# Kernel tuning notes

Hardware: AMD Instinct MI355X
Metric: run time of the kernel (lower is better)

Reference implementation:

```python
import jax, jax.numpy as jnp
import numpy as np

B, S, C, H, D = 2, 2048, 1024, 16, 64  # hidden C must equal H*D (value is a reshape of key_states)


def setup_inputs() -> dict:
    key = jax.random.key(0)
    ks = jax.random.split(key, 7)
    query_states = jax.random.normal(ks[0], (B, S, C), dtype=jnp.float32)
    key_states = jax.random.normal(ks[1], (B, S, C), dtype=jnp.float32)
    attention_mask = jax.random.randint(ks[2], (B, 1, 1, S), 0, 2).astype(jnp.int32)
    Wq = jax.random.normal(ks[3], (C, H, D), dtype=jnp.float32) * 0.02
    bq = jnp.zeros((H, D), dtype=jnp.float32)
    Wk = jax.random.normal(ks[4], (C, H, D), dtype=jnp.float32) * 0.02
    bk = jnp.zeros((H, D), dtype=jnp.float32)
    return {
        "query_states": query_states,
        "key_states": key_states,
        "attention_mask": attention_mask,
        "Wq": Wq,
        "bq": bq,
        "Wk": Wk,
        "bk": bk,
    }


def reference(query_states, key_states, attention_mask, Wq, bq, Wk, bk):
    # EinsumDense 'abc,cde->abde' with bias on 'de'
    q = jnp.einsum("bsc,chd->bshd", query_states, Wq) + bq  # [B,S,H,D]
    k = jnp.einsum("bsc,chd->bshd", key_states, Wk) + bk    # [B,S,H,D]
    # value is just key_states reshaped into head layout (no projection!)
    v = key_states.reshape(k.shape)                          # [B,S,H,D]
    # scale query by 1/sqrt(dk)
    q = q * jax.lax.rsqrt(jnp.asarray(D, q.dtype))
    # 'aecd,abcd->acbe': a=batch, c=head, b=query pos, e=key pos
    scores = jnp.einsum("bkhd,bqhd->bhqk", k, q)             # [B,H,Sq,Sk]
    mask = (1.0 - attention_mask.astype(scores.dtype)) * -10000.0
    scores = scores + mask
    probs = jax.nn.softmax(scores, axis=-1)
    # dropout is identity at training=False (default)
    # 'acbe,aecd->abcd': weighted sum of values over key positions
    out = jnp.einsum("bhqk,bkhd->bqhd", probs, v)            # [B,S,H,D]
    return out
```

## Files before the change

### kernel.cpp

```cpp
#include <hip/hip_runtime.h>

#define BSZ 2
#define SEQ 2048
#define CH  1024
#define NH  16
#define HD  64
#define LOG2E 1.4426950408889634f
#define MASKC (-14426.950408889634f)

typedef short  bf16x8 __attribute__((ext_vector_type(8)));
typedef short  bf16x4 __attribute__((ext_vector_type(4)));
typedef float  f32x4  __attribute__((ext_vector_type(4)));

__device__ __forceinline__ short f2bf(float f) {
    union { float f; unsigned u; } v; v.f = f;
    unsigned r = v.u + 0x7FFFu + ((v.u >> 16) & 1u);
    return (short)(r >> 16);
}
__device__ __forceinline__ short f2bf_fast(float f) {
    union { float f; unsigned u; } v; v.f = f;
    return (short)((v.u + 0x8000u) >> 16);
}
__device__ __forceinline__ float exp2_hw(float x) {
#if __has_builtin(__builtin_amdgcn_exp2f)
    return __builtin_amdgcn_exp2f(x);
#else
    float r;
    asm volatile("v_exp_f32 %0, %1\n\ts_nop 1" : "=v"(r) : "v"(x));
    return r;
#endif
}

#if __has_builtin(__builtin_amdgcn_mfma_f32_16x16x16bf16_1k)
__device__ __forceinline__ f32x4 mfma16x16x16(bf16x4 a, bf16x4 b, f32x4 c) {
    return __builtin_amdgcn_mfma_f32_16x16x16bf16_1k(a, b, c, 0, 0, 0);
}
#else
__device__ __forceinline__ f32x4 mfma16x16x16(bf16x4 a, bf16x4 b, f32x4 c) {
    f32x4 d;
    asm("v_mfma_f32_16x16x16_bf16 %0, %1, %2, %3"
        : "=v"(d) : "v"(a), "v"(b), "v"(c));
    return d;
}
#endif

__global__ __launch_bounds__(256) void prep(
    const float* __restrict__ query, const float* __restrict__ key,
    const float* __restrict__ Wq, const float* __restrict__ Wk,
    short* __restrict__ qc, short* __restrict__ kc,
    short* __restrict__ wtq, short* __restrict__ wtk,
    short* __restrict__ vtr)
{
    __shared__ float tile[64][65];
    const int bid = blockIdx.x;
    const int tid = threadIdx.x;

    if (bid < 4096) {
        const float* s = (bid < 2048) ? query : key;
        short*       d = (bid < 2048) ? qc : kc;
        long i = ((long)(bid & 2047) * 256 + tid) * 8;
        float4 v0 = *(const float4*)&s[i];
        float4 v1 = *(const float4*)&s[i + 4];
        bf16x8 o;
        o[0] = f2bf(v0.x); o[1] = f2bf(v0.y); o[2] = f2bf(v0.z); o[3] = f2bf(v0.w);
        o[4] = f2bf(v1.x); o[5] = f2bf(v1.y); o[6] = f2bf(v1.z); o[7] = f2bf(v1.w);
        *(bf16x8*)&d[i] = o;
        return;
    }

    const float* s; short* d;
    int r0, c0, srs, drs;
    if (bid < 4608) {
        int t = bid - 4096;
        s   = (t < 256) ? Wq : Wk;
        d   = (t < 256) ? wtq : wtk;
        t  &= 255;
        r0  = (t >> 4) * 64;
        c0  = (t & 15) * 64;
        srs = CH; drs = CH;
    } else {
        int t = bid - 4608;
        int z = t >> 5;
        int sy = t & 31;
        s   = key + (long)(z >> 4) * SEQ * CH + (long)(z & 15) * HD;
        d   = vtr + (long)z * HD * SEQ;
        r0  = sy * 64;
        c0  = 0;
        srs = CH; drs = SEQ;
    }

    const int r  = tid >> 2;
    const int c4 = (tid & 3) << 4;
    #pragma unroll
    for (int i = 0; i < 16; i += 4) {
        float4 v = *(const float4*)&s[(long)(r0 + r) * srs + c0 + c4 + i];
        tile[r][c4 + i + 0] = v.x;
        tile[r][c4 + i + 1] = v.y;
        tile[r][c4 + i + 2] = v.z;
        tile[r][c4 + i + 3] = v.w;
    }
    __syncthreads();
    bf16x8 o0, o1;
    #pragma unroll
    for (int i = 0; i < 8; i++) o0[i] = f2bf(tile[c4 + i][r]);
    #pragma unroll
    for (int i = 0; i < 8; i++) o1[i] = f2bf(tile[c4 + 8 + i][r]);
    *(bf16x8*)&d[(long)(c0 + r) * drs + r0 + c4 + 0] = o0;
    *(bf16x8*)&d[(long)(c0 + r) * drs + r0 + c4 + 8] = o1;
}

__global__ __launch_bounds__(256, 2) void proj_mfma(
    const short* __restrict__ Xq, const short* __restrict__ Xk,
    const short* __restrict__ Wtq, const short* __restrict__ Wtk,
    const float* __restrict__ bq_, const float* __restrict__ bk_,
    short* __restrict__ Yq, short* __restrict__ Yk)
{
    __shared__ short At[2][128 * 72];
    __shared__ short Bt[2][128 * 72];
    const int zz = blockIdx.z;
    const short* X    = zz ? Xk  : Xq;
    const short* Wt   = zz ? Wtk : Wtq;
    const float* bias = zz ? bk_ : bq_;
    short*       Y    = zz ? Yk  : Yq;
    const float scale = zz ? 1.0f : (0.125f * LOG2E);

    const int tid  = threadIdx.x;
    const int lane = tid & 63, w = tid >> 6;
    const int quad = lane >> 4, t16 = lane & 15;
    const int m0 = blockIdx.y * 128, n0 = blockIdx.x * 128;
    const int srow = tid >> 1;
    const int shalf = (tid & 1) * 32;

    f32x4 acc[4][4];
    #pragma unroll
    for (int i = 0; i < 4; i++)
        #pragma unroll
        for (int j = 0; j < 4; j++)
            acc[i][j] = (f32x4){0.f, 0.f, 0.f, 0.f};

    const int M0 = (w >> 1) * 64, N0 = (w & 1) * 64;
    const int NIT = CH / 64;

    bf16x8 ar[4], br[4];
    #pragma unroll
    for (int c = 0; c < 4; c++) {
        ar[c] = *(const bf16x8*)&X [(long)(m0 + srow) * CH + shalf + 8 * c];
        br[c] = *(const bf16x8*)&Wt[(long)(n0 + srow) * CH + shalf + 8 * c];
    }
    #pragma unroll
    for (int c = 0; c < 4; c++) {
        *(bf16x8*)&At[0][srow * 72 + shalf + 8 * c] = ar[c];
        *(bf16x8*)&Bt[0][srow * 72 + shalf + 8 * c] = br[c];
    }
    #pragma unroll
    for (int c = 0; c < 4; c++) {
        ar[c] = *(const bf16x8*)&X [(long)(m0 + srow) * CH + 64 + shalf + 8 * c];
        br[c] = *(const bf16x8*)&Wt[(long)(n0 + srow) * CH + 64 + shalf + 8 * c];
    }
    __syncthreads();

    for (int it = 0; it < NIT; it++) {
        const int buf = it & 1;
        if (it + 1 < NIT) {
            #pragma unroll
            for (int c = 0; c < 4; c++) {
                *(bf16x8*)&At[buf ^ 1][srow * 72 + shalf + 8 * c] = ar[c];
                *(bf16x8*)&Bt[buf ^ 1][srow * 72 + shalf + 8 * c] = br[c];
            }
            if (it + 2 < NIT) {
                const long ko = (long)(it + 2) * 64;
                #pragma unroll
                for (int c = 0; c < 4; c++) {
                    ar[c] = *(const bf16x8*)&X [(long)(m0 + srow) * CH + ko + shalf + 8 * c];
                    br[c] = *(const bf16x8*)&Wt[(long)(n0 + srow) * CH + ko + shalf + 8 * c];
                }
            }
        }

        #pragma unroll
        for (int kk = 0; kk < 2; kk++) {
            bf16x8 af[4], bw[4];
            #pragma unroll
            for (int im = 0; im < 4; im++)
                af[im] = *(bf16x8*)&At[buf][(M0 + 16 * im + t16) * 72 + kk * 32 + quad * 8];
            #pragma unroll
            for (int jn = 0; jn < 4; jn++)
                bw[jn] = *(bf16x8*)&Bt[buf][(N0 + 16 * jn + t16) * 72 + kk * 32 + quad * 8];
            #pragma unroll
            for (int im = 0; im < 4; im++)
                #pragma unroll
                for (int jn = 0; jn < 4; jn++)
                    acc[im][jn] = __builtin_amdgcn_mfma_f32_16x16x32_bf16(
                        af[im], bw[jn], acc[im][jn], 0, 0, 0);
        }
        __syncthreads();
    }

    #pragma unroll
    for (int jn = 0; jn < 4; jn++) {
        float bs = bias[n0 + N0 + 16 * jn + t16];
        #pragma unroll
        for (int im = 0; im < 4; im++)
            #pragma unroll
            for (int reg = 0; reg < 4; reg++) {
                float y = (acc[im][jn][reg] + bs) * scale;
                Y[(long)(m0 + M0 + 16 * im + 4 * quad + reg) * (NH * HD)
                  + n0 + N0 + 16 * jn + t16] = f2bf(y);
            }
    }
}

__global__ __launch_bounds__(256, 2) void attn_mfma(
    const short* __restrict__ qp,
    const short* __restrict__ kp,
    const short* __restrict__ vt,
    const int*   __restrict__ amask,
    float* __restrict__ out)
{
    __shared__ short Kt[2][64 * 72];
    __shared__ short Vt[2][64 * 72];

    const int qt0 = blockIdx.x * 128;
    const int h   = blockIdx.y;
    const int b   = blockIdx.z;
    const int tid = threadIdx.x;
    const int lane = tid & 63, w = tid >> 6;
    const int quad = lane >> 4, t16 = lane & 15;

    bf16x8 qf[2][2];
    #pragma unroll
    for (int qm = 0; qm < 2; qm++)
        #pragma unroll
        for (int ds = 0; ds < 2; ds++)
            qf[qm][ds] = *(const bf16x8*)&qp[
                (long)(b * SEQ + qt0 + w * 32 + qm * 16 + t16) * CH
                + h * HD + ds * 32 + quad * 8];

    f32x4 oa[4][2];
    float l_r[2];
    #pragma unroll
    for (int dt = 0; dt < 4; dt++)
        #pragma unroll
        for (int qm = 0; qm < 2; qm++)
            oa[dt][qm] = (f32x4){0.f, 0.f, 0.f, 0.f};
    l_r[0] = l_r[1] = 0.f;

    const int srow  = tid >> 2;
    const int scol  = (tid & 3) * 16;
    const long kbase = (long)(b * SEQ) * CH + h * HD;
    const long vbase = ((long)(b * NH + h) * HD) * SEQ;
    const int NIT = SEQ / 64;

    bf16x8 kr[2], vr[2];
    #pragma unroll
    for (int c = 0; c < 2; c++) {
        kr[c] = *(const bf16x8*)&kp[kbase + (long)srow * CH + scol + 8 * c];
        vr[c] = *(const bf16x8*)&vt[vbase + (long)srow * SEQ + scol + 8 * c];
    }
    #pragma unroll
    for (int c = 0; c < 2; c++) {
        *(bf16x8*)&Kt[0][srow * 72 + scol + 8 * c] = kr[c];
        *(bf16x8*)&Vt[0][srow * 72 + scol + 8 * c] = vr[c];
    }
    #pragma unroll
    for (int c = 0; c < 2; c++) {
        kr[c] = *(const bf16x8*)&kp[kbase + (long)(64 + srow) * CH + scol + 8 * c];
        vr[c] = *(const bf16x8*)&vt[vbase + (long)srow * SEQ + 64 + scol + 8 * c];
    }
    __syncthreads();

    for (int it = 0; it < NIT; it++) {
        const int buf = it & 1;
        const int kt0 = it * 64;

        if (it + 1 < NIT) {
            #pragma unroll
            for (int c = 0; c < 2; c++) {
                *(bf16x8*)&Kt[buf ^ 1][srow * 72 + scol + 8 * c] = kr[c];
                *(bf16x8*)&Vt[buf ^ 1][srow * 72 + scol + 8 * c] = vr[c];
            }
            if (it + 2 < NIT) {
                const int kn = kt0 + 128;
                #pragma unroll
                for (int c = 0; c < 2; c++) {
                    kr[c] = *(const bf16x8*)&kp[kbase + (long)(kn + srow) * CH + scol + 8 * c];
                    vr[c] = *(const bf16x8*)&vt[vbase + (long)srow * SEQ + kn + scol + 8 * c];
                }
            }
        }

        float4 mv4[4];
        #pragma unroll
        for (int jt = 0; jt < 4; jt++) {
            int4 a4 = *(const int4*)&amask[b * SEQ + kt0 + jt * 16 + quad * 4];
            mv4[jt].x = a4.x ? 0.f : MASKC;
            mv4[jt].y = a4.y ? 0.f : MASKC;
            mv4[jt].z = a4.z ? 0.f : MASKC;
            mv4[jt].w = a4.w ? 0.f : MASKC;
        }

        f32x4 sa[2][4];
        #pragma unroll
        for (int qm = 0; qm < 2; qm++)
            #pragma unroll
            for (int jt = 0; jt < 4; jt++)
                sa[qm][jt] = (f32x4){mv4[jt].x, mv4[jt].y, mv4[jt].z, mv4[jt].w};
        #pragma unroll
        for (int ds = 0; ds < 2; ds++) {
            bf16x8 kb[4];
            #pragma unroll
            for (int jt = 0; jt < 4; jt++)
                kb[jt] = *(bf16x8*)&Kt[buf][(jt * 16 + t16) * 72 + ds * 32 + quad * 8];
            #pragma unroll
            for (int qm = 0; qm < 2; qm++)
                #pragma unroll
                for (int jt = 0; jt < 4; jt++)
                    sa[qm][jt] = __builtin_amdgcn_mfma_f32_16x16x32_bf16(
                        kb[jt], qf[qm][ds], sa[qm][jt], 0, 0, 0);
        }

        bf16x4 pb[2][4];
        #pragma unroll
        for (int qm = 0; qm < 2; qm++)
            #pragma unroll
            for (int jt = 0; jt < 4; jt++) {
                float p0 = exp2_hw(sa[qm][jt][0]);
                float p1 = exp2_hw(sa[qm][jt][1]);
                float p2 = exp2_hw(sa[qm][jt][2]);
                float p3 = exp2_hw(sa[qm][jt][3]);
                l_r[qm] += (p0 + p1) + (p2 + p3);
                bf16x4 pk;
                pk[0] = f2bf_fast(p0); pk[1] = f2bf_fast(p1);
                pk[2] = f2bf_fast(p2); pk[3] = f2bf_fast(p3);
                pb[qm][jt] = pk;
            }

        #pragma unroll
        for (int jt = 0; jt < 4; jt++) {
            bf16x4 va[4];
            #pragma unroll
            for (int dt = 0; dt < 4; dt++)
                va[dt] = *(bf16x4*)&Vt[buf][(dt * 16 + t16) * 72 + jt * 16 + quad * 4];
            #pragma unroll
            for (int dt = 0; dt < 4; dt++)
                #pragma unroll
                for (int qm = 0; qm < 2; qm++)
                    oa[dt][qm] = mfma16x16x16(va[dt], pb[qm][jt], oa[dt][qm]);
        }
        __syncthreads();
    }

    #pragma unroll
    for (int qm = 0; qm < 2; qm++) {
        float l = l_r[qm];
        l += __shfl_xor(l, 16, 64);
        l += __shfl_xor(l, 32, 64);
        float inv = 1.0f / l;
        int q = qt0 + w * 32 + qm * 16 + t16;
        #pragma unroll
        for (int dt = 0; dt < 4; dt++) {
            f32x4 o = oa[dt][qm];
            float4 st = {o[0] * inv, o[1] * inv, o[2] * inv, o[3] * inv};
            *(float4*)&out[((long)(b * SEQ + q) * NH + h) * HD + dt * 16 + quad * 4] = st;
        }
    }
}

extern "C" void kernel_launch(void* const* d_in, const int* in_sizes, int n_in,
                              void* d_out, int out_size, void* d_ws, size_t ws_size,
                              hipStream_t stream) {
    const float* query = (const float*)d_in[0];
    const float* key   = (const float*)d_in[1];
    const int*   amask = (const int*)d_in[2];
    const float* Wq    = (const float*)d_in[3];
    const float* bq    = (const float*)d_in[4];
    const float* Wk    = (const float*)d_in[5];
    const float* bk    = (const float*)d_in[6];
    float* out = (float*)d_out;

    char* ws = (char*)d_ws;
    const long MB = 1024 * 1024;
    short* qc  = (short*)(ws + 0 * MB);
    short* kc  = (short*)(ws + 8 * MB);
    short* qp  = (short*)(ws + 16 * MB);
    short* kp  = (short*)(ws + 24 * MB);
    short* vtr = (short*)(ws + 32 * MB);
    short* wtq = (short*)(ws + 40 * MB);
    short* wtk = (short*)(ws + 42 * MB);

    prep<<<dim3(5632), 256, 0, stream>>>(query, key, Wq, Wk, qc, kc, wtq, wtk, vtr);

    dim3 pgrid((NH * HD) / 128, (BSZ * SEQ) / 128, 2);
    proj_mfma<<<pgrid, 256, 0, stream>>>(qc, kc, wtq, wtk, bq, bk, qp, kp);

    dim3 agrid(SEQ / 128, NH, BSZ);
    attn_mfma<<<agrid, 256, 0, stream>>>(qp, kp, vtr, amask, out);
}
```

Measured before the change: 174.8 us.

## Fuse fp32-to-bf16 input conversion into projection GEMM and precompute float mask

```diff
diff --git a/kernel.cpp b/kernel.cpp
--- a/kernel.cpp
+++ b/kernel.cpp
@@ -20,6 +20,12 @@
 __device__ __forceinline__ short f2bf_fast(float f) {
     union { float f; unsigned u; } v; v.f = f;
     return (short)((v.u + 0x8000u) >> 16);
+}
+__device__ __forceinline__ bf16x8 pack8(float4 a, float4 b) {
+    bf16x8 o;
+    o[0] = f2bf(a.x); o[1] = f2bf(a.y); o[2] = f2bf(a.z); o[3] = f2bf(a.w);
+    o[4] = f2bf(b.x); o[5] = f2bf(b.y); o[6] = f2bf(b.z); o[7] = f2bf(b.w);
+    return o;
 }
 __device__ __forceinline__ float exp2_hw(float x) {
 #if __has_builtin(__builtin_amdgcn_exp2f)
@@ -45,33 +51,26 @@
 #endif
 
 __global__ __launch_bounds__(256) void prep(
-    const float* __restrict__ query, const float* __restrict__ key,
+    const float* __restrict__ key,
     const float* __restrict__ Wq, const float* __restrict__ Wk,
-    short* __restrict__ qc, short* __restrict__ kc,
+    const int*   __restrict__ am,
     short* __restrict__ wtq, short* __restrict__ wtk,
-    short* __restrict__ vtr)
+    short* __restrict__ vtr, float* __restrict__ mf)
 {
     __shared__ float tile[64][65];
     const int bid = blockIdx.x;
     const int tid = threadIdx.x;
 
-    if (bid < 4096) {
-        const float* s = (bid < 2048) ? query : key;
-        short*       d = (bid < 2048) ? qc : kc;
-        long i = ((long)(bid & 2047) * 256 + tid) * 8;
-        float4 v0 = *(const float4*)&s[i];
-        float4 v1 = *(const float4*)&s[i + 4];
-        bf16x8 o;
-        o[0] = f2bf(v0.x); o[1] = f2bf(v0.y); o[2] = f2bf(v0.z); o[3] = f2bf(v0.w);
-        o[4] = f2bf(v1.x); o[5] = f2bf(v1.y); o[6] = f2bf(v1.z); o[7] = f2bf(v1.w);
-        *(bf16x8*)&d[i] = o;
+    if (bid >= 1536) {
+        int i = (bid - 1536) * 256 + tid;
+        mf[i] = (1.0f - (float)am[i]) * MASKC * (1.0f / 1.0f);
         return;
     }
 
     const float* s; short* d;
     int r0, c0, srs, drs;
-    if (bid < 4608) {
-        int t = bid - 4096;
+    if (bid < 512) {
+        int t = bid;
         s   = (t < 256) ? Wq : Wk;
         d   = (t < 256) ? wtq : wtk;
         t  &= 255;
@@ -79,7 +78,7 @@
         c0  = (t & 15) * 64;
         srs = CH; drs = CH;
     } else {
-        int t = bid - 4608;
+        int t = bid - 512;
         int z = t >> 5;
         int sy = t & 31;
         s   = key + (long)(z >> 4) * SEQ * CH + (long)(z & 15) * HD;
@@ -110,7 +109,7 @@
 }
 
 __global__ __launch_bounds__(256, 2) void proj_mfma(
-    const short* __restrict__ Xq, const short* __restrict__ Xk,
+    const float* __restrict__ Xq, const float* __restrict__ Xk,
     const short* __restrict__ Wtq, const short* __restrict__ Wtk,
     const float* __restrict__ bq_, const float* __restrict__ bk_,
     short* __restrict__ Yq, short* __restrict__ Yk)
@@ -118,7 +117,7 @@
     __shared__ short At[2][128 * 72];
     __shared__ short Bt[2][128 * 72];
     const int zz = blockIdx.z;
-    const short* X    = zz ? Xk  : Xq;
+    const float* X    = zz ? Xk  : Xq;
     const short* Wt   = zz ? Wtk : Wtq;
     const float* bias = zz ? bk_ : bq_;
     short*       Y    = zz ? Yk  : Yq;
@@ -141,22 +140,25 @@
     const int M0 = (w >> 1) * 64, N0 = (w & 1) * 64;
     const int NIT = CH / 64;
 
-    bf16x8 ar[4], br[4];
+    float4 xr[8];
+    bf16x8 br[4];
+    #pragma unroll
+    for (int c = 0; c < 8; c++)
+        xr[c] = *(const float4*)&X[(long)(m0 + srow) * CH + shalf + 4 * c];
+    #pragma unroll
+    for (int c = 0; c < 4; c++)
+        br[c] = *(const bf16x8*)&Wt[(long)(n0 + srow) * CH + shalf + 8 * c];
     #pragma unroll
     for (int c = 0; c < 4; c++) {
-        ar[c] = *(const bf16x8*)&X [(long)(m0 + srow) * CH + shalf + 8 * c];
-        br[c] = *(const bf16x8*)&Wt[(long)(n0 + srow) * CH + shalf + 8 * c];
-    }
-    #pragma unroll
-    for (int c = 0; c < 4; c++) {
-        *(bf16x8*)&At[0][srow * 72 + shalf + 8 * c] = ar[c];
+        *(bf16x8*)&At[0][srow * 72 + shalf + 8 * c] = pack8(xr[2 * c], xr[2 * c + 1]);
         *(bf16x8*)&Bt[0][srow * 72 + shalf + 8 * c] = br[c];
     }
     #pragma unroll
-    for (int c = 0; c < 4; c++) {
-        ar[c] = *(const bf16x8*)&X [(long)(m0 + srow) * CH + 64 + shalf + 8 * c];
+    for (int c = 0; c < 8; c++)
+        xr[c] = *(const float4*)&X[(long)(m0 + srow) * CH + 64 + shalf + 4 * c];
+    #pragma unroll
+    for (int c = 0; c < 4; c++)
         br[c] = *(const bf16x8*)&Wt[(long)(n0 + srow) * CH + 64 + shalf + 8 * c];
-    }
     __syncthreads();
 
     for (int it = 0; it < NIT; it++) {
@@ -164,16 +166,17 @@
         if (it + 1 < NIT) {
             #pragma unroll
             for (int c = 0; c < 4; c++) {
-                *(bf16x8*)&At[buf ^ 1][srow * 72 + shalf + 8 * c] = ar[c];
+                *(bf16x8*)&At[buf ^ 1][srow * 72 + shalf + 8 * c] = pack8(xr[2 * c], xr[2 * c + 1]);
                 *(bf16x8*)&Bt[buf ^ 1][srow * 72 + shalf + 8 * c] = br[c];
             }
             if (it + 2 < NIT) {
                 const long ko = (long)(it + 2) * 64;
                 #pragma unroll
-                for (int c = 0; c < 4; c++) {
-                    ar[c] = *(const bf16x8*)&X [(long)(m0 + srow) * CH + ko + shalf + 8 * c];
+                for (int c = 0; c < 8; c++)
+                    xr[c] = *(const float4*)&X[(long)(m0 + srow) * CH + ko + shalf + 4 * c];
+                #pragma unroll
+                for (int c = 0; c < 4; c++)
                     br[c] = *(const bf16x8*)&Wt[(long)(n0 + srow) * CH + ko + shalf + 8 * c];
-                }
             }
         }
 
@@ -214,7 +217,7 @@
     const short* __restrict__ qp,
     const short* __restrict__ kp,
     const short* __restrict__ vt,
-    const int*   __restrict__ amask,
+    const float* __restrict__ mf,
     float* __restrict__ out)
 {
     __shared__ short Kt[2][64 * 72];
@@ -291,13 +294,8 @@
 
         float4 mv4[4];
         #pragma unroll
-        for (int jt = 0; jt < 4; jt++) {
-            int4 a4 = *(const int4*)&amask[b * SEQ + kt0 + jt * 16 + quad * 4];
-            mv4[jt].x = a4.x ? 0.f : MASKC;
-            mv4[jt].y = a4.y ? 0.f : MASKC;
-            mv4[jt].z = a4.z ? 0.f : MASKC;
-            mv4[jt].w = a4.w ? 0.f : MASKC;
-        }
+        for (int jt = 0; jt < 4; jt++)
+            mv4[jt] = *(const float4*)&mf[b * SEQ + kt0 + jt * 16 + quad * 4];
 
         f32x4 sa[2][4];
         #pragma unroll
@@ -380,19 +378,18 @@
 
     char* ws = (char*)d_ws;
     const long MB = 1024 * 1024;
-    short* qc  = (short*)(ws + 0 * MB);
-    short* kc  = (short*)(ws + 8 * MB);
-    short* qp  = (short*)(ws + 16 * MB);
-    short* kp  = (short*)(ws + 24 * MB);
-    short* vtr = (short*)(ws + 32 * MB);
-    short* wtq = (short*)(ws + 40 * MB);
-    short* wtk = (short*)(ws + 42 * MB);
-
-    prep<<<dim3(5632), 256, 0, stream>>>(query, key, Wq, Wk, qc, kc, wtq, wtk, vtr);
+    short* qp  = (short*)(ws + 0 * MB);
+    short* kp  = (short*)(ws + 8 * MB);
+    short* vtr = (short*)(ws + 16 * MB);
+    short* wtq = (short*)(ws + 24 * MB);
+    short* wtk = (short*)(ws + 26 * MB);
+    float* mfv = (float*)(ws + 28 * MB);
+
+    prep<<<dim3(1552), 256, 0, stream>>>(key, Wq, Wk, amask, wtq, wtk, vtr, mfv);
 
     dim3 pgrid((NH * HD) / 128, (BSZ * SEQ) / 128, 2);
-    proj_mfma<<<pgrid, 256, 0, stream>>>(qc, kc, wtq, wtk, bq, bk, qp, kp);
+    proj_mfma<<<pgrid, 256, 0, stream>>>(query, key, wtq, wtk, bq, bk, qp, kp);
 
     dim3 agrid(SEQ / 128, NH, BSZ);
-    attn_mfma<<<agrid, 256, 0, stream>>>(qp, kp, vtr, amask, out);
-}
+    attn_mfma<<<agrid, 256, 0, stream>>>(qp, kp, vtr, mfv, out);
+}
```

Measured after the change: 192.5 us. 1.1x slower.

## Split attention key range across two blocks and reduce partial outputs

Applied to the files above, without the earlier changes.

```diff
diff --git a/kernel.cpp b/kernel.cpp
--- a/kernel.cpp
+++ b/kernel.cpp
@@ -47,9 +47,10 @@
 __global__ __launch_bounds__(256) void prep(
     const float* __restrict__ query, const float* __restrict__ key,
     const float* __restrict__ Wq, const float* __restrict__ Wk,
+    const int*   __restrict__ am,
     short* __restrict__ qc, short* __restrict__ kc,
     short* __restrict__ wtq, short* __restrict__ wtk,
-    short* __restrict__ vtr)
+    short* __restrict__ vtr, float* __restrict__ mf)
 {
     __shared__ float tile[64][65];
     const int bid = blockIdx.x;
@@ -65,6 +66,11 @@
         o[0] = f2bf(v0.x); o[1] = f2bf(v0.y); o[2] = f2bf(v0.z); o[3] = f2bf(v0.w);
         o[4] = f2bf(v1.x); o[5] = f2bf(v1.y); o[6] = f2bf(v1.z); o[7] = f2bf(v1.w);
         *(bf16x8*)&d[i] = o;
+        return;
+    }
+    if (bid >= 5632) {
+        int i = (bid - 5632) * 256 + tid;
+        mf[i] = (1.0f - (float)am[i]) * MASKC;
         return;
     }
 
@@ -210,22 +216,29 @@
     }
 }
 
-__global__ __launch_bounds__(256, 2) void attn_mfma(
+__global__ __launch_bounds__(256, 4) void attn_mfma(
     const short* __restrict__ qp,
     const short* __restrict__ kp,
     const short* __restrict__ vt,
-    const int*   __restrict__ amask,
-    float* __restrict__ out)
+    const float* __restrict__ mf,
+    float* __restrict__ out,
+    float* __restrict__ opA,
+    float* __restrict__ opB,
+    float* __restrict__ lp,
+    int nkh)
 {
     __shared__ short Kt[2][64 * 72];
     __shared__ short Vt[2][64 * 72];
 
     const int qt0 = blockIdx.x * 128;
     const int h   = blockIdx.y;
-    const int b   = blockIdx.z;
+    const int b   = blockIdx.z / nkh;
+    const int kh  = blockIdx.z - b * nkh;
     const int tid = threadIdx.x;
     const int lane = tid & 63, w = tid >> 6;
     const int quad = lane >> 4, t16 = lane & 15;
+    const int NIT = (SEQ / 64) / nkh;
+    const int khbase = kh * (SEQ / nkh);
 
     bf16x8 qf[2][2];
     #pragma unroll
@@ -249,13 +262,12 @@
     const int scol  = (tid & 3) * 16;
     const long kbase = (long)(b * SEQ) * CH + h * HD;
     const long vbase = ((long)(b * NH + h) * HD) * SEQ;
-    const int NIT = SEQ / 64;
 
     bf16x8 kr[2], vr[2];
     #pragma unroll
     for (int c = 0; c < 2; c++) {
-        kr[c] = *(const bf16x8*)&kp[kbase + (long)srow * CH + scol + 8 * c];
-        vr[c] = *(const bf16x8*)&vt[vbase + (long)srow * SEQ + scol + 8 * c];
+        kr[c] = *(const bf16x8*)&kp[kbase + (long)(khbase + srow) * CH + scol + 8 * c];
+        vr[c] = *(const bf16x8*)&vt[vbase + (long)srow * SEQ + khbase + scol + 8 * c];
     }
     #pragma unroll
     for (int c = 0; c < 2; c++) {
@@ -264,14 +276,14 @@
     }
     #pragma unroll
     for (int c = 0; c < 2; c++) {
-        kr[c] = *(const bf16x8*)&kp[kbase + (long)(64 + srow) * CH + scol + 8 * c];
-        vr[c] = *(const bf16x8*)&vt[vbase + (long)srow * SEQ + 64 + scol + 8 * c];
+        kr[c] = *(const bf16x8*)&kp[kbase + (long)(khbase + 64 + srow) * CH + scol + 8 * c];
+        vr[c] = *(const bf16x8*)&vt[vbase + (long)srow * SEQ + khbase + 64 + scol + 8 * c];
     }
     __syncthreads();
 
     for (int it = 0; it < NIT; it++) {
         const int buf = it & 1;
-        const int kt0 = it * 64;
+        const int kt0 = khbase + it * 64;
 
         if (it + 1 < NIT) {
             #pragma unroll
@@ -291,13 +303,8 @@
 
         float4 mv4[4];
         #pragma unroll
-        for (int jt = 0; jt < 4; jt++) {
-            int4 a4 = *(const int4*)&amask[b * SEQ + kt0 + jt * 16 + quad * 4];
-            mv4[jt].x = a4.x ? 0.f : MASKC;
-            mv4[jt].y = a4.y ? 0.f : MASKC;
-            mv4[jt].z = a4.z ? 0.f : MASKC;
-            mv4[jt].w = a4.w ? 0.f : MASKC;
-        }
+        for (int jt = 0; jt < 4; jt++)
+            mv4[jt] = *(const float4*)&mf[b * SEQ + kt0 + jt * 16 + quad * 4];
 
         f32x4 sa[2][4];
         #pragma unroll
@@ -355,15 +362,42 @@
         float l = l_r[qm];
         l += __shfl_xor(l, 16, 64);
         l += __shfl_xor(l, 32, 64);
-        float inv = 1.0f / l;
         int q = qt0 + w * 32 + qm * 16 + t16;
-        #pragma unroll
-        for (int dt = 0; dt < 4; dt++) {
-            f32x4 o = oa[dt][qm];
-            float4 st = {o[0] * inv, o[1] * inv, o[2] * inv, o[3] * inv};
-            *(float4*)&out[((long)(b * SEQ + q) * NH + h) * HD + dt * 16 + quad * 4] = st;
-        }
-    }
+        long row = (long)(b * SEQ + q) * NH + h;
+        if (nkh == 1) {
+            float inv = 1.0f / l;
+            #pragma unroll
+            for (int dt = 0; dt < 4; dt++) {
+                f32x4 o = oa[dt][qm];
+                float4 st = {o[0] * inv, o[1] * inv, o[2] * inv, o[3] * inv};
+                *(float4*)&out[row * HD + dt * 16 + quad * 4] = st;
+            }
+        } else {
+            float* op = kh ? opB : opA;
+            if (quad == 0) lp[(long)kh * (BSZ * SEQ * NH) + row] = l;
+            #pragma unroll
+            for (int dt = 0; dt < 4; dt++) {
+                f32x4 o = oa[dt][qm];
+                float4 st = {o[0], o[1], o[2], o[3]};
+                *(float4*)&op[row * HD + dt * 16 + quad * 4] = st;
+            }
+        }
+    }
+}
+
+__global__ __launch_bounds__(256) void reduce_split(
+    const float* __restrict__ o0, const float* __restrict__ o1,
+    const float* __restrict__ lp, float* __restrict__ out)
+{
+    long i4 = (long)blockIdx.x * 256 + threadIdx.x;
+    long e  = i4 * 4;
+    long row = i4 >> 4;
+    float4 a = *(const float4*)&o0[e];
+    float4 b = *(const float4*)&o1[e];
+    float inv = 1.0f / (lp[row] + lp[(long)(BSZ * SEQ * NH) + row]);
+    float4 o = {(a.x + b.x) * inv, (a.y + b.y) * inv,
+                (a.z + b.z) * inv, (a.w + b.w) * inv};
+    *(float4*)&out[e] = o;
 }
 
 extern "C" void kernel_launch(void* const* d_in, const int* in_sizes, int n_in,
@@ -387,12 +421,25 @@
     short* vtr = (short*)(ws + 32 * MB);
     short* wtq = (short*)(ws + 40 * MB);
     short* wtk = (short*)(ws + 42 * MB);
-
-    prep<<<dim3(5632), 256, 0, stream>>>(query, key, Wq, Wk, qc, kc, wtq, wtk, vtr);
+    float* mfv = (float*)(ws + 44 * MB);
+    float* opA = (float*)(ws + 0 * MB);
+    float* opB = (float*)(ws + 45 * MB);
+    float* lpp = (float*)(ws + 61 * MB);
+
+    const bool split = ws_size >= (size_t)(62 * MB);
+    const int  nkh   = split ? 2 : 1;
+
+    prep<<<dim3(5648), 256, 0, stream>>>(query, key, Wq, Wk, amask,
+                                         qc, kc, wtq, wtk, vtr, mfv);
 
     dim3 pgrid((NH * HD) / 128, (BSZ * SEQ) / 128, 2);
     proj_mfma<<<pgrid, 256, 0, stream>>>(qc, kc, wtq, wtk, bq, bk, qp, kp);
 
-    dim3 agrid(SEQ / 128, NH, BSZ);
-    attn_mfma<<<agrid, 256, 0, stream>>>(qp, kp, vtr, amask, out);
-}
+    dim3 agrid(SEQ / 128, NH, BSZ * nkh);
+    attn_mfma<<<agrid, 256, 0, stream>>>(qp, kp, vtr, mfv, out,
+                                         opA, opB, lpp, nkh);
+
+    if (split) {
+        reduce_split<<<dim3(4096), 256, 0, stream>>>(opA, opB, lpp, out);
+    }
+}
```

After: 209.8 us. 1.2x slower.
